# Kernel optimization log

Measured on AMD Instinct MI355X. Metric: run time of the kernel, lower is better.

The kernel has to match this reference:

```python
import jax, jax.numpy as jnp
import numpy as np

HOP = 128
NFFT = 256
SR = 16000
EPS = 1e-7
MIN_DB = -80.0


def _a_weighting_db():
    # librosa.fft_frequencies + librosa.A_weighting (min_db=-80), computed statically in numpy
    f = np.fft.rfftfreq(NFFT, d=1.0 / SR)  # [NFFT//2+1]
    c = np.array([12194.217, 20.598997, 107.65265, 737.86223]) ** 2.0
    f2 = f ** 2.0
    w = 2.0 + 20.0 * (
        np.log10(c[0])
        + 2.0 * np.log10(np.maximum(f2, 1e-30))
        - np.log10(f2 + c[0])
        - np.log10(f2 + c[1])
        - 0.5 * np.log10(f2 + c[2])
        - 0.5 * np.log10(f2 + c[3])
    )
    return np.maximum(w, MIN_DB).astype(np.float32)


def _loudness(x):
    # x: [B, C, T] -> channel mean -> librosa-style centered STFT (hann, reflect pad)
    x = jnp.mean(x, axis=1)  # [B, T]
    T = x.shape[1]
    pad = NFFT // 2
    xp = jnp.pad(x, ((0, 0), (pad, pad)), mode='reflect')  # [B, T+NFFT]
    n_frames = 1 + T // HOP
    idx = jnp.arange(n_frames)[:, None] * HOP + jnp.arange(NFFT)[None, :]  # [F, NFFT]
    frames = xp[:, idx]  # [B, F, NFFT]
    # periodic hann window (scipy fftbins=True, librosa default)
    win = (0.5 - 0.5 * jnp.cos(2.0 * jnp.pi * jnp.arange(NFFT) / NFFT)).astype(x.dtype)
    spec = jnp.fft.rfft(frames * win, axis=-1)  # [B, F, NFFT//2+1] complex
    log_mag = jnp.log(jnp.abs(spec) + EPS)  # [B, F, NFREQ]
    aw = jnp.asarray(_a_weighting_db())  # [NFREQ]
    # mean over frequency axis, then trailing singleton like original unsqueeze(-1)
    loud = jnp.mean(log_mag + aw[None, None, :], axis=-1)  # [B, F]
    return loud[..., None].astype(jnp.float32)


def setup_inputs() -> dict:
    key = jax.random.key(0)
    x = jax.random.normal(key, (64, 1, 640000), dtype=jnp.float32)
    return {"x": x}


def reference(x):
    return _loudness(x)
```

## Files before the change

### kernel.cpp

```cpp
#include <hip/hip_runtime.h>
#include <math.h>

#define HOP 128
#define T_LEN 640000
#define N_FRAMES 5001
#define N_PAIRS 2501
#define NB 64
#define GPB 16

typedef float v2f __attribute__((ext_vector_type(2)));

static __device__ __forceinline__ v2f mk2(float a, float b) { v2f r; r.x = a; r.y = b; return r; }
static __device__ __forceinline__ v2f sp(float s) { v2f r; r.x = s; r.y = s; return r; }

__global__ __launch_bounds__(256) void loudness_kernel(const float* __restrict__ x,
                                                       float* __restrict__ out) {
    constexpr float C16[16] = {
        1.0f,  0.9238795325112867f,  0.7071067811865476f,  0.3826834323650898f,
        0.0f, -0.3826834323650898f, -0.7071067811865476f, -0.9238795325112867f,
       -1.0f, -0.9238795325112867f, -0.7071067811865476f, -0.3826834323650898f,
        0.0f,  0.3826834323650898f,  0.7071067811865476f,  0.9238795325112867f};
    constexpr float S16[16] = {
        0.0f,  0.3826834323650898f,  0.7071067811865476f,  0.9238795325112867f,
        1.0f,  0.9238795325112867f,  0.7071067811865476f,  0.3826834323650898f,
        0.0f, -0.3826834323650898f, -0.7071067811865476f, -0.9238795325112867f,
       -1.0f, -0.9238795325112867f, -0.7071067811865476f, -0.3826834323650898f};
    const float R2  = 0.7071067811865476f;
    const float c1v = 0.9238795325112867f, s1v = 0.3826834323650898f;
    const float c3v = 0.3826834323650898f, s3v = 0.9238795325112867f;

    __shared__ float4 s_c[GPB][145];
    __shared__ float  s_winT[256];
    __shared__ v2f    s_twP[256];
    __shared__ float  s_aw8[16];
    __shared__ float  s_aw128;

    const int tid = threadIdx.x;

    {
        const int hi = tid >> 4, lo = tid & 15;
        const float TP = 0.02454369260617026f;
        s_winT[tid] = 0.5f - 0.5f * cosf((float)(hi + 16 * lo) * TP);
        float s, c;
        sincosf((float)(hi * lo) * TP, &s, &c);
        s_twP[tid] = mk2(c, -s);
        if (tid < 129) {
            float fq = (float)tid * 62.5f;
            float f2 = fq * fq;
            const float a0 = 12194.217f * 12194.217f;
            const float a1 = 20.598997f * 20.598997f;
            const float a2 = 107.65265f * 107.65265f;
            const float a3 = 737.86223f * 737.86223f;
            float w = 2.0f + 20.0f * (log10f(a0) + 2.0f * log10f(fmaxf(f2, 1e-30f))
                     - log10f(f2 + a0) - log10f(f2 + a1)
                     - 0.5f * log10f(f2 + a2) - 0.5f * log10f(f2 + a3));
            ((float*)&s_c[0][0])[tid] = fmaxf(w, -80.0f);
        }
    }
    __syncthreads();
    if (tid < 16) {
        const float* scr = (const float*)&s_c[0][0];
        float s = 0.f;
#pragma unroll
        for (int k2 = 0; k2 < 8; ++k2) s += scr[tid + 16 * k2];
        s_aw8[tid] = s;
        if (tid == 0) s_aw128 = scr[128];
    }
    __syncthreads();

    const int g  = tid >> 4;
    const int r  = tid & 15;
    const int gp = blockIdx.x * GPB + g;
    const int b  = gp / N_PAIRS;
    const int pp = gp - b * N_PAIRS;
    const int fA = 2 * pp;
    const int fB = (fA < 5000) ? fA + 1 : 5000;
    const int dB = (fB - fA) * HOP;
    const float* __restrict__ xb = x + (size_t)b * T_LEN;

    v2f xw[16];
    const int base = fA * HOP - HOP + r;
    const float4* __restrict__ winr = (const float4*)&s_winT[r * 16];
    if (pp >= 1 && pp <= 2499) {
        const float* __restrict__ xp = xb + base;
#pragma unroll
        for (int c4 = 0; c4 < 4; ++c4) {
            const float4 wq = winr[c4];
            const int o = 64 * c4;
            xw[4 * c4 + 0] = mk2(xp[o +  0], xp[o +  0 + dB]) * sp(wq.x);
            xw[4 * c4 + 1] = mk2(xp[o + 16], xp[o + 16 + dB]) * sp(wq.y);
            xw[4 * c4 + 2] = mk2(xp[o + 32], xp[o + 32 + dB]) * sp(wq.z);
            xw[4 * c4 + 3] = mk2(xp[o + 48], xp[o + 48 + dB]) * sp(wq.w);
        }
    } else {
#pragma unroll
        for (int c4 = 0; c4 < 4; ++c4) {
            const float4 wq = winr[c4];
            const float wv[4] = {wq.x, wq.y, wq.z, wq.w};
#pragma unroll
            for (int e = 0; e < 4; ++e) {
                const int n2 = 4 * c4 + e;
                int jA = base + 16 * n2;
                int jB = jA + dB;
                jA = (jA < 0) ? -jA : jA;
                jA = (jA >= T_LEN) ? (2 * T_LEN - 2 - jA) : jA;
                jB = (jB < 0) ? -jB : jB;
                jB = (jB >= T_LEN) ? (2 * T_LEN - 2 - jB) : jB;
                xw[n2] = mk2(xb[jA], xb[jB]) * sp(wv[e]);
            }
        }
    }

    v2f p[8], q[8];
#pragma unroll
    for (int n = 1; n <= 7; ++n) { p[n] = xw[n] + xw[16 - n]; q[n] = xw[n] - xw[16 - n]; }
    const v2f bse = xw[0] + xw[8];
    const v2f d08 = xw[0] - xw[8];
    const v2f se  = p[2] + p[4] + p[6];
    const v2f so  = p[1] + p[3] + p[5] + p[7];
    const v2f r0  = bse + se + so;
    const v2f r8  = bse + se - so;
    v2f rre[8], rim[8];
#pragma unroll
    for (int k1 = 1; k1 <= 7; ++k1) {
        v2f re = (k1 & 1) ? d08 : bse;
        v2f im = sp(0.f);
#pragma unroll
        for (int n = 1; n <= 7; ++n) {
            const int m = (k1 * n) & 15;
            re += p[n] * sp(C16[m]);
            im -= q[n] * sp(S16[m]);
        }
        rre[k1] = re;
        rim[k1] = im;
    }

    float4* __restrict__ myrow = &s_c[g][r * 9];
    myrow[0] = make_float4(r0.x, r0.y, 0.f, 0.f);
#pragma unroll
    for (int k = 1; k <= 7; ++k)
        myrow[k] = make_float4(rre[k].x, rre[k].y, rim[k].x, rim[k].y);
    myrow[8] = make_float4(r8.x, r8.y, 0.f, 0.f);
    __syncthreads();

    const int rp = (r <= 8) ? r : 16 - r;
    const v2f sgnv = sp((r <= 8) ? 1.f : -1.f);
    const v2f* __restrict__ twr = &s_twP[r * 16];
    const float4* __restrict__ col = &s_c[g][rp];
    v2f bbx[16], bby[16];
#pragma unroll
    for (int w = 0; w < 16; ++w) {
        const float4 fv = col[w * 9];
        const v2f xx = mk2(fv.x, fv.y);
        const v2f yy = mk2(fv.z, fv.w) * sgnv;
        const v2f t = twr[w];
        bbx[w] = xx * sp(t.x) - yy * sp(t.y);
        bby[w] = xx * sp(t.y) + yy * sp(t.x);
    }

#pragma unroll
    for (int j = 0; j < 8; ++j) {
        const v2f ux = bbx[j], uy = bby[j], vx = bbx[j + 8], vy = bby[j + 8];
        bbx[j] = ux + vx; bby[j] = uy + vy;
        const v2f dx = ux - vx, dy = uy - vy;
        v2f ox, oy;
        if      (j == 0) { ox = dx;                              oy = dy; }
        else if (j == 1) { ox =  dx * sp(c1v) + dy * sp(s1v);    oy =  dy * sp(c1v) - dx * sp(s1v); }
        else if (j == 2) { ox = (dx + dy) * sp(R2);              oy = (dy - dx) * sp(R2); }
        else if (j == 3) { ox =  dx * sp(c3v) + dy * sp(s3v);    oy =  dy * sp(c3v) - dx * sp(s3v); }
        else if (j == 4) { ox = dy;                              oy = sp(0.f) - dx; }
        else if (j == 5) { ox = dy * sp(s3v) - dx * sp(c3v);     oy = sp(0.f) - dy * sp(c3v) - dx * sp(s3v); }
        else if (j == 6) { ox = (dy - dx) * sp(R2);              oy = sp(0.f) - (dx + dy) * sp(R2); }
        else             { ox = dy * sp(s1v) - dx * sp(c1v);     oy = sp(0.f) - dy * sp(c1v) - dx * sp(s1v); }
        bbx[j + 8] = ox; bby[j + 8] = oy;
    }
#pragma unroll
    for (int h = 0; h <= 8; h += 8) {
#pragma unroll
        for (int j = 0; j < 4; ++j) {
            const v2f ux = bbx[h + j], uy = bby[h + j], vx = bbx[h + j + 4], vy = bby[h + j + 4];
            bbx[h + j] = ux + vx; bby[h + j] = uy + vy;
            const v2f dx = ux - vx, dy = uy - vy;
            v2f ox, oy;
            if      (j == 0) { ox = dx;                  oy = dy; }
            else if (j == 1) { ox = (dx + dy) * sp(R2);  oy = (dy - dx) * sp(R2); }
            else if (j == 2) { ox = dy;                  oy = sp(0.f) - dx; }
            else             { ox = (dy - dx) * sp(R2);  oy = sp(0.f) - (dx + dy) * sp(R2); }
            bbx[h + j + 4] = ox; bby[h + j + 4] = oy;
        }
    }
#pragma unroll
    for (int gg = 0; gg < 16; gg += 4) {
        {
            const v2f ux = bbx[gg], uy = bby[gg], vx = bbx[gg + 2], vy = bby[gg + 2];
            bbx[gg] = ux + vx;     bby[gg] = uy + vy;
            bbx[gg + 2] = ux - vx; bby[gg + 2] = uy - vy;
        }
        {
            const v2f ux = bbx[gg + 1], uy = bby[gg + 1], vx = bbx[gg + 3], vy = bby[gg + 3];
            bbx[gg + 1] = ux + vx; bby[gg + 1] = uy + vy;
            const v2f dx = ux - vx, dy = uy - vy;
            bbx[gg + 3] = dy; bby[gg + 3] = sp(0.f) - dx;
        }
    }

    const float HALF_LN2 = 0.34657359027997264f;
    v2f m2[8];
#pragma unroll
    for (int t = 0; t < 8; ++t) {
        const v2f Yx = bbx[2 * t] + bbx[2 * t + 1];
        const v2f Yy = bby[2 * t] + bby[2 * t + 1];
        m2[t] = Yx * Yx + Yy * Yy + sp(1e-14f);
    }
    const v2f P0 = m2[0] * m2[1], P1 = m2[2] * m2[3], P2 = m2[4] * m2[5], P3 = m2[6] * m2[7];
    const float lA = __builtin_amdgcn_logf(P0.x) + __builtin_amdgcn_logf(P1.x)
                   + __builtin_amdgcn_logf(P2.x) + __builtin_amdgcn_logf(P3.x);
    const float lB = __builtin_amdgcn_logf(P0.y) + __builtin_amdgcn_logf(P1.y)
                   + __builtin_amdgcn_logf(P2.y) + __builtin_amdgcn_logf(P3.y);
    v2f ssum = sp(HALF_LN2) * mk2(lA, lB) + sp(s_aw8[r]);

    const v2f d0 = bbx[0] - bbx[1];
    if (r == 0) {
        ssum += sp(HALF_LN2) * mk2(__builtin_amdgcn_logf(d0.x * d0.x + 1e-14f),
                                   __builtin_amdgcn_logf(d0.y * d0.y + 1e-14f))
              + sp(s_aw128);
    }

    ssum.x += __shfl_xor(ssum.x, 1); ssum.y += __shfl_xor(ssum.y, 1);
    ssum.x += __shfl_xor(ssum.x, 2); ssum.y += __shfl_xor(ssum.y, 2);
    ssum.x += __shfl_xor(ssum.x, 4); ssum.y += __shfl_xor(ssum.y, 4);
    ssum.x += __shfl_xor(ssum.x, 8); ssum.y += __shfl_xor(ssum.y, 8);

    if (r == 0) {
        out[b * N_FRAMES + fA] = ssum.x * (1.0f / 129.0f);
        out[b * N_FRAMES + fB] = ssum.y * (1.0f / 129.0f);
    }
}

extern "C" void kernel_launch(void* const* d_in, const int* in_sizes, int n_in,
                              void* d_out, int out_size, void* d_ws, size_t ws_size,
                              hipStream_t stream) {
    const float* x = (const float*)d_in[0];
    float* out = (float*)d_out;
    loudness_kernel<<<(NB * N_PAIRS) / GPB, 256, 0, stream>>>(x, out);
}
```

Baseline: 65.30 us.

## Split FFT exchange into padded re/im LDS arrays, compute twiddles in registers

Splits the shared-memory transpose buffer into separate real and imaginary arrays with padded strides so the second FFT stage reads float4 pairs of adjacent columns. Window and twiddle tables are no longer stored in LDS; they are generated per thread with a Chebyshev cosine recurrence and complex rotation. The 16-lane reduction switches from shuffles to DPP row operations. This cuts LDS traffic and table setup, at the cost of extra ALU work, a small accumulated rounding error from the recurrences, and an added zero-fill and barrier.

```diff
diff --git a/kernel.cpp b/kernel.cpp
--- a/kernel.cpp
+++ b/kernel.cpp
@@ -8,10 +8,23 @@
 #define NB 64
 #define GPB 16
 
+#define RE_SLOT 18
+#define RE_GRP  160
+#define IM_SLOT 18
+#define IM_GRP  142
+
 typedef float v2f __attribute__((ext_vector_type(2)));
 
 static __device__ __forceinline__ v2f mk2(float a, float b) { v2f r; r.x = a; r.y = b; return r; }
 static __device__ __forceinline__ v2f sp(float s) { v2f r; r.x = s; r.y = s; return r; }
+
+static __device__ __forceinline__ float rsum16(float v) {
+    v += __int_as_float(__builtin_amdgcn_update_dpp(0, __float_as_int(v), 0xB1, 0xF, 0xF, true));
+    v += __int_as_float(__builtin_amdgcn_update_dpp(0, __float_as_int(v), 0x4E, 0xF, 0xF, true));
+    v += __int_as_float(__builtin_amdgcn_update_dpp(0, __float_as_int(v), 0x141, 0xF, 0xF, true));
+    v += __int_as_float(__builtin_amdgcn_update_dpp(0, __float_as_int(v), 0x140, 0xF, 0xF, true));
+    return v;
+}
 
 __global__ __launch_bounds__(256) void loudness_kernel(const float* __restrict__ x,
                                                        float* __restrict__ out) {
@@ -28,22 +41,24 @@
     const float R2  = 0.7071067811865476f;
     const float c1v = 0.9238795325112867f, s1v = 0.3826834323650898f;
     const float c3v = 0.3826834323650898f, s3v = 0.9238795325112867f;
-
-    __shared__ float4 s_c[GPB][145];
-    __shared__ float  s_winT[256];
-    __shared__ v2f    s_twP[256];
-    __shared__ float  s_aw8[16];
-    __shared__ float  s_aw128;
+    const float CP8 = 0.9238795325112867f, SP8 = 0.3826834323650898f;
+    const float K2  = 1.8477590650225735f;
+
+    __shared__ alignas(16) v2f s_re[16 * RE_GRP];
+    __shared__ alignas(16) v2f s_im[16 * IM_GRP];
+    __shared__ v2f   s_stp[16];
+    __shared__ float s_aw8[16];
+    __shared__ float s_aw128;
 
     const int tid = threadIdx.x;
 
     {
-        const int hi = tid >> 4, lo = tid & 15;
         const float TP = 0.02454369260617026f;
-        s_winT[tid] = 0.5f - 0.5f * cosf((float)(hi + 16 * lo) * TP);
-        float s, c;
-        sincosf((float)(hi * lo) * TP, &s, &c);
-        s_twP[tid] = mk2(c, -s);
+        if (tid < 16) {
+            float s, c;
+            sincosf((float)tid * TP, &s, &c);
+            s_stp[tid] = mk2(c, -s);
+        }
         if (tid < 129) {
             float fq = (float)tid * 62.5f;
             float f2 = fq * fq;
@@ -54,18 +69,20 @@
             float w = 2.0f + 20.0f * (log10f(a0) + 2.0f * log10f(fmaxf(f2, 1e-30f))
                      - log10f(f2 + a0) - log10f(f2 + a1)
                      - 0.5f * log10f(f2 + a2) - 0.5f * log10f(f2 + a3));
-            ((float*)&s_c[0][0])[tid] = fmaxf(w, -80.0f);
+            ((float*)&s_im[0])[tid] = fmaxf(w, -80.0f);
         }
     }
     __syncthreads();
     if (tid < 16) {
-        const float* scr = (const float*)&s_c[0][0];
+        const float* scr = (const float*)&s_im[0];
         float s = 0.f;
 #pragma unroll
         for (int k2 = 0; k2 < 8; ++k2) s += scr[tid + 16 * k2];
         s_aw8[tid] = s;
         if (tid == 0) s_aw128 = scr[128];
     }
+    __syncthreads();
+    s_im[(tid >> 4) * IM_GRP + (tid & 15)] = sp(0.f);
     __syncthreads();
 
     const int g  = tid >> 4;
@@ -78,36 +95,40 @@
     const int dB = (fB - fA) * HOP;
     const float* __restrict__ xb = x + (size_t)b * T_LEN;
 
+    const v2f stp = s_stp[r];
+    float win16[16];
+    {
+        float cm2 = stp.x;
+        float cm1 = stp.x * CP8 + stp.y * SP8;
+        win16[0] = 0.5f - 0.5f * cm2;
+        win16[1] = 0.5f - 0.5f * cm1;
+#pragma unroll
+        for (int n = 2; n < 16; ++n) {
+            const float c = K2 * cm1 - cm2;
+            win16[n] = 0.5f - 0.5f * c;
+            cm2 = cm1; cm1 = c;
+        }
+    }
+
     v2f xw[16];
     const int base = fA * HOP - HOP + r;
-    const float4* __restrict__ winr = (const float4*)&s_winT[r * 16];
     if (pp >= 1 && pp <= 2499) {
         const float* __restrict__ xp = xb + base;
 #pragma unroll
-        for (int c4 = 0; c4 < 4; ++c4) {
-            const float4 wq = winr[c4];
-            const int o = 64 * c4;
-            xw[4 * c4 + 0] = mk2(xp[o +  0], xp[o +  0 + dB]) * sp(wq.x);
-            xw[4 * c4 + 1] = mk2(xp[o + 16], xp[o + 16 + dB]) * sp(wq.y);
-            xw[4 * c4 + 2] = mk2(xp[o + 32], xp[o + 32 + dB]) * sp(wq.z);
-            xw[4 * c4 + 3] = mk2(xp[o + 48], xp[o + 48 + dB]) * sp(wq.w);
+        for (int n2 = 0; n2 < 16; ++n2) {
+            const int o = 16 * n2;
+            xw[n2] = mk2(xp[o], xp[o + dB]) * sp(win16[n2]);
         }
     } else {
 #pragma unroll
-        for (int c4 = 0; c4 < 4; ++c4) {
-            const float4 wq = winr[c4];
-            const float wv[4] = {wq.x, wq.y, wq.z, wq.w};
-#pragma unroll
-            for (int e = 0; e < 4; ++e) {
-                const int n2 = 4 * c4 + e;
-                int jA = base + 16 * n2;
-                int jB = jA + dB;
-                jA = (jA < 0) ? -jA : jA;
-                jA = (jA >= T_LEN) ? (2 * T_LEN - 2 - jA) : jA;
-                jB = (jB < 0) ? -jB : jB;
-                jB = (jB >= T_LEN) ? (2 * T_LEN - 2 - jB) : jB;
-                xw[n2] = mk2(xb[jA], xb[jB]) * sp(wv[e]);
-            }
+        for (int n2 = 0; n2 < 16; ++n2) {
+            int jA = base + 16 * n2;
+            int jB = jA + dB;
+            jA = (jA < 0) ? -jA : jA;
+            jA = (jA >= T_LEN) ? (2 * T_LEN - 2 - jA) : jA;
+            jB = (jB < 0) ? -jB : jB;
+            jB = (jB >= T_LEN) ? (2 * T_LEN - 2 - jB) : jB;
+            xw[n2] = mk2(xb[jA], xb[jB]) * sp(win16[n2]);
         }
     }
 
@@ -135,27 +156,54 @@
         rim[k1] = im;
     }
 
-    float4* __restrict__ myrow = &s_c[g][r * 9];
-    myrow[0] = make_float4(r0.x, r0.y, 0.f, 0.f);
-#pragma unroll
-    for (int k = 1; k <= 7; ++k)
-        myrow[k] = make_float4(rre[k].x, rre[k].y, rim[k].x, rim[k].y);
-    myrow[8] = make_float4(r8.x, r8.y, 0.f, 0.f);
-    __syncthreads();
-
-    const int rp = (r <= 8) ? r : 16 - r;
+    {
+        v2f* __restrict__ reW = &s_re[g * RE_GRP + r];
+        v2f* __restrict__ imW = &s_im[g * IM_GRP + r];
+        reW[0] = r0;
+#pragma unroll
+        for (int k = 1; k <= 7; ++k) {
+            reW[RE_SLOT * k] = rre[k];
+            imW[IM_SLOT * k] = rim[k];
+        }
+        reW[RE_SLOT * 8] = r8;
+    }
+
+    const int rp  = (r <= 8) ? r : 16 - r;
+    const int rp7 = rp & 7;
     const v2f sgnv = sp((r <= 8) ? 1.f : -1.f);
-    const v2f* __restrict__ twr = &s_twP[r * 16];
-    const float4* __restrict__ col = &s_c[g][rp];
+    const float4* __restrict__ reCol = (const float4*)&s_re[g * RE_GRP + RE_SLOT * rp];
+    const float4* __restrict__ imCol = (const float4*)&s_im[g * IM_GRP + IM_SLOT * rp7];
+
     v2f bbx[16], bby[16];
-#pragma unroll
-    for (int w = 0; w < 16; ++w) {
-        const float4 fv = col[w * 9];
-        const v2f xx = mk2(fv.x, fv.y);
-        const v2f yy = mk2(fv.z, fv.w) * sgnv;
-        const v2f t = twr[w];
-        bbx[w] = xx * sp(t.x) - yy * sp(t.y);
-        bby[w] = xx * sp(t.y) + yy * sp(t.x);
+    float tc = 1.f, tms = 0.f;
+    const float sc = stp.x, sms = stp.y;
+#pragma unroll
+    for (int j = 0; j < 8; ++j) {
+        const float4 R4v = reCol[j];
+        const float4 I4v = imCol[j];
+        {
+            const v2f xx = mk2(R4v.x, R4v.y);
+            const v2f yy = mk2(I4v.x, I4v.y) * sgnv;
+            if (j == 0) { bbx[0] = xx; bby[0] = yy; }
+            else {
+                bbx[2 * j] = xx * sp(tc) - yy * sp(tms);
+                bby[2 * j] = xx * sp(tms) + yy * sp(tc);
+            }
+            const float ntc = tc * sc - tms * sms;
+            const float nts = tc * sms + tms * sc;
+            tc = ntc; tms = nts;
+        }
+        {
+            const v2f xx = mk2(R4v.z, R4v.w);
+            const v2f yy = mk2(I4v.z, I4v.w) * sgnv;
+            bbx[2 * j + 1] = xx * sp(tc) - yy * sp(tms);
+            bby[2 * j + 1] = xx * sp(tms) + yy * sp(tc);
+            if (j < 7) {
+                const float ntc = tc * sc - tms * sms;
+                const float nts = tc * sms + tms * sc;
+                tc = ntc; tms = nts;
+            }
+        }
     }
 
 #pragma unroll
@@ -226,10 +274,8 @@
               + sp(s_aw128);
     }
 
-    ssum.x += __shfl_xor(ssum.x, 1); ssum.y += __shfl_xor(ssum.y, 1);
-    ssum.x += __shfl_xor(ssum.x, 2); ssum.y += __shfl_xor(ssum.y, 2);
-    ssum.x += __shfl_xor(ssum.x, 4); ssum.y += __shfl_xor(ssum.y, 4);
-    ssum.x += __shfl_xor(ssum.x, 8); ssum.y += __shfl_xor(ssum.y, 8);
+    ssum.x = rsum16(ssum.x);
+    ssum.y = rsum16(ssum.y);
 
     if (r == 0) {
         out[b * N_FRAMES + fA] = ssum.x * (1.0f / 129.0f);
```

Measured after the change: 57.14 us. -12.5%, faster.
